# Optimization experiments

Measured on AMD Instinct MI355X. Metric: run time of the kernel, lower is better.

## Reference

```python
import jax, jax.numpy as jnp
import numpy as np

B, F, V, D, K = 16384, 39, 30000, 16, 20
EPS = 1e-5


def bn_eval(x, g, b):
    # inference-mode BatchNorm1d with running_mean=0, running_var=1
    return g * x / jnp.sqrt(1.0 + EPS) + b


def setup_inputs() -> dict:
    key = jax.random.key(0)
    ks = jax.random.split(key, 12)
    x = jax.random.randint(ks[0], (B, F), 0, V)
    emb_table = jax.random.normal(ks[1], (F * V, D), dtype=jnp.float32) * 0.05
    w_c = jax.random.normal(ks[2], (F, F * D), dtype=jnp.float32) * 0.05
    w0 = jax.random.normal(ks[3], (1024, F * D), dtype=jnp.float32) * 0.04
    w1 = jax.random.normal(ks[4], (512, 1024), dtype=jnp.float32) * 0.03
    w_out = jax.random.normal(ks[5], (1, 512), dtype=jnp.float32) * 0.04
    return {
        'x': x, 'emb_table': emb_table,
        'w_c': w_c, 'b_c': jnp.zeros((F,)), 'g_c': jnp.ones((F,)), 'be_c': jnp.zeros((F,)),
        'w0': w0, 'b0': jnp.zeros((1024,)), 'g0': jnp.ones((1024,)), 'be0': jnp.zeros((1024,)),
        'w1': w1, 'b1': jnp.zeros((512,)), 'g1': jnp.ones((512,)), 'be1': jnp.zeros((512,)),
        'w_out': w_out, 'b_out': jnp.zeros((1,)),
    }


def reference(x, emb_table, w_c, b_c, g_c, be_c, w0, b0, g0, be0,
              w1, b1, g1, be1, w_out, b_out):
    offsets = jnp.arange(F, dtype=x.dtype) * V          # per-field offsets
    idx = x + offsets[None, :]                          # [B, F]
    emb = emb_table[idx]                                # [B, F, D] gather

    # controller_mlp: flatten (batch, D, F) layout like torch transpose(1,2)
    flat = jnp.transpose(emb, (0, 2, 1)).reshape(B, F * D)
    h = jax.nn.relu(bn_eval(flat @ w_c.T + b_c, g_c, be_c))
    scores = jax.nn.softmax(h, axis=1)                  # [B, F]

    # kmax_pooling: top-k field indices, sorted ascending, gather weights
    _, kidx = jax.lax.top_k(scores, K)
    kidx = jnp.sort(kidx, axis=1)                       # [B, K]
    w = jnp.take_along_axis(scores, kidx, axis=1)       # [B, K]

    # forward_select: gather selected field embeddings, weight them
    sel = jnp.take_along_axis(emb, kidx[:, :, None], axis=1)  # [B, K, D]
    weighted = sel * w[:, :, None]

    # scatter back into full field slots (unselected fields are zero)
    full = jnp.zeros((B, F, D), weighted.dtype)
    bidx = jnp.arange(B)[:, None]
    full = full.at[bidx, kidx].set(weighted)            # [B, F, D]

    z = jnp.transpose(full, (0, 2, 1)).reshape(B, F * D)
    z = jax.nn.relu(bn_eval(z @ w0.T + b0, g0, be0))
    z = jax.nn.relu(bn_eval(z @ w1.T + b1, g1, be1))
    out = jax.nn.sigmoid(z @ w_out.T + b_out)           # [B, 1]
    return out.squeeze(-1)
```

## Files before the change

kernel.cpp:

```cpp
#include <hip/hip_runtime.h>
#include <math.h>

#define B_SZ 16384
#define F_N 39
#define V_N 30000
#define D_N 16
#define K_SEL 20
#define FD 624
#define KP0 640
#define NCP 64
#define N0 1024
#define N1 512
#define WSL 40

typedef unsigned short u16;
typedef __attribute__((ext_vector_type(8))) short bf16x8;
typedef __attribute__((ext_vector_type(4))) float f32x4;
typedef __attribute__((ext_vector_type(4))) unsigned short u16x4;

__device__ __forceinline__ u16 f2bf(float v) {
    union { float f; unsigned u; } x; x.f = v;
    unsigned r = x.u + 0x7fff + ((x.u >> 16) & 1);
    return (u16)(r >> 16);
}
__device__ __forceinline__ float bf2f(u16 v) {
    union { unsigned u; float f; } x; x.u = ((unsigned)v) << 16;
    return x.f;
}

#define GLD16(gp, lp) __builtin_amdgcn_global_load_lds( \
    (const __attribute__((address_space(1))) unsigned int*)(gp), \
    (__attribute__((address_space(3))) unsigned int*)(lp), 16, 0, 0)

__global__ void convert_kernel(const float* __restrict__ src, u16* __restrict__ dst,
                               int n_el)
{
    int i = blockIdx.x * blockDim.x + threadIdx.x;
    if (i < n_el) dst[i] = f2bf(src[i]);
}

__global__ void prep_w0_kernel(const float* __restrict__ w0, u16* __restrict__ w0p)
{
    int i = blockIdx.x * blockDim.x + threadIdx.x;
    if (i >= N0 * KP0) return;
    int n = i / KP0, kk = i - n * KP0;
    float v = 0.f;
    if (kk < FD) {
        int f = kk >> 4, d = kk & 15;
        v = w0[n * FD + d * F_N + f];
    }
    w0p[i] = f2bf(v);
}

__global__ void prep_wc_kernel(const float* __restrict__ w_c, u16* __restrict__ wcb)
{
    int i = blockIdx.x * blockDim.x + threadIdx.x;
    if (i >= NCP * KP0) return;
    int n = i / KP0, kk = i - n * KP0;
    float v = 0.f;
    if (n < F_N && kk < FD) {
        int f = kk >> 4, d = kk & 15;
        v = w_c[n * FD + d * F_N + f];
    }
    wcb[i] = f2bf(v);
}

__global__ void pad_params_kernel(const float* __restrict__ b_c,
                                  const float* __restrict__ g_c,
                                  const float* __restrict__ be_c,
                                  float* __restrict__ bp, float* __restrict__ gp,
                                  float* __restrict__ bep)
{
    int n = threadIdx.x;
    bp[n]  = (n < F_N) ? b_c[n]  : 0.f;
    gp[n]  = (n < F_N) ? g_c[n]  : 0.f;
    bep[n] = (n < F_N) ? be_c[n] : 0.f;
}

#define GROWS_BLK 64
#define GBLOCKS (B_SZ * F_N / GROWS_BLK)
__global__ __launch_bounds__(256) void gather_kernel(
    const int* __restrict__ x, const float* __restrict__ emb_table,
    u16* __restrict__ flatb)
{
    const int t = threadIdx.x;
    if (blockIdx.x >= GBLOCKS) {
        int b = (blockIdx.x - GBLOCKS) * 256 + t;
        float4 zz = {0.f, 0.f, 0.f, 0.f};
        float4* p = (float4*)(flatb + (size_t)b * KP0 + FD);
        p[0] = zz; p[1] = zz;
        return;
    }
    const int r = blockIdx.x * GROWS_BLK + (t >> 2);
    const int lane4 = t & 3;
    const int b = r / F_N;
    const int f = r - b * F_N;
    const int row = x[r] + f * V_N;
    const float4 v = *(const float4*)(emb_table + (size_t)row * D_N + lane4 * 4);
    u16x4 o = { f2bf(v.x), f2bf(v.y), f2bf(v.z), f2bf(v.w) };
    *(u16x4*)(flatb + (size_t)b * KP0 + f * D_N + lane4 * 4) = o;
}

__global__ __launch_bounds__(256) void controller_gemm_select_kernel(
    const u16* __restrict__ A, const u16* __restrict__ W,
    const float* __restrict__ bias, const float* __restrict__ g,
    const float* __restrict__ be, float* __restrict__ wsel)
{
    __shared__ __align__(16) u16 As[64 * 32];
    __shared__ __align__(16) u16 Bs[64 * 32];
    __shared__ float vv[64][65];

    const int t    = threadIdx.x;
    const int wave = t >> 6;
    const int lane = t & 63;
    const int m0   = blockIdx.x * 64;

    const int lr    = lane >> 2;
    const int swz_u = (lane & 3) ^ ((lane >> 3) & 3);
    const u16* gA = A + (size_t)(m0 + wave * 16 + lr) * KP0 + swz_u * 8;
    const u16* gB = W + (size_t)(wave * 16 + lr) * KP0 + swz_u * 8;
    u16* lA = &As[(wave * 16) * 32];
    u16* lB = &Bs[(wave * 16) * 32];

    const int q    = lane >> 4;
    const int lr16 = lane & 15;

    const int ra = wave * 16 + lr16;
    const int aoff = ra * 32 + ((q ^ ((ra >> 1) & 3)) * 8);
    int boff[4];
    #pragma unroll
    for (int j = 0; j < 4; ++j) {
        int rb = j * 16 + lr16;
        boff[j] = rb * 32 + ((q ^ ((rb >> 1) & 3)) * 8);
    }

    f32x4 acc[4] = {};

    for (int k0 = 0; k0 < KP0; k0 += 32) {
        GLD16(gA, lA); GLD16(gB, lB);
        gA += 32; gB += 32;
        __syncthreads();
        bf16x8 af = *(const bf16x8*)&As[aoff];
        bf16x8 bfr[4];
        #pragma unroll
        for (int j = 0; j < 4; ++j) bfr[j] = *(const bf16x8*)&Bs[boff[j]];
        #pragma unroll
        for (int j = 0; j < 4; ++j)
            acc[j] = __builtin_amdgcn_mfma_f32_16x16x32_bf16(af, bfr[j], acc[j], 0, 0, 0);
        __syncthreads();
    }

    const float rs = rsqrtf(1.0f + 1e-5f);
    #pragma unroll
    for (int j = 0; j < 4; ++j) {
        const int n = j * 16 + lr16;
        const float bn_g = g[n] * rs;
        const float bn_b = be[n];
        const float bi   = bias[n];
        #pragma unroll
        for (int r = 0; r < 4; ++r) {
            float v = acc[j][r] + bi;
            vv[wave * 16 + q * 4 + r][n] = fmaxf(fmaf(bn_g, v, bn_b), 0.f);
        }
    }
    __syncthreads();

    if (t < 64) {
        float rv[F_N];
        #pragma unroll
        for (int f = 0; f < F_N; ++f) rv[f] = vv[t][f];
        float mx = rv[0];
        #pragma unroll
        for (int f = 1; f < F_N; ++f) mx = fmaxf(mx, rv[f]);
        float sum = 0.f;
        #pragma unroll
        for (int f = 0; f < F_N; ++f) { rv[f] = expf(rv[f] - mx); sum += rv[f]; }
        const float inv = 1.f / sum;
        float* wrow = wsel + (size_t)(m0 + t) * WSL;
        #pragma unroll
        for (int f = 0; f < F_N; ++f) {
            int rank = 0;
            #pragma unroll
            for (int gg = 0; gg < F_N; ++gg)
                rank += (rv[gg] > rv[f] || (rv[gg] == rv[f] && gg < f)) ? 1 : 0;
            wrow[f] = (rank < K_SEL) ? rv[f] * inv : 0.f;
        }
    }
}

__global__ __launch_bounds__(256) void select_scale_kernel(
    const u16* __restrict__ flatb, const float* __restrict__ wsel,
    u16* __restrict__ zb)
{
    const int i = blockIdx.x * blockDim.x + threadIdx.x;
    const int b = i / (KP0 / 8);
    const int kk = (i - b * (KP0 / 8)) * 8;
    u16x4 o0 = {0, 0, 0, 0}, o1 = {0, 0, 0, 0};
    if (kk < FD) {
        const float s = wsel[(size_t)b * WSL + (kk >> 4)];
        const u16x4* src = (const u16x4*)(flatb + (size_t)b * KP0 + kk);
        u16x4 a0 = src[0], a1 = src[1];
        o0 = { f2bf(bf2f(a0.x) * s), f2bf(bf2f(a0.y) * s),
               f2bf(bf2f(a0.z) * s), f2bf(bf2f(a0.w) * s) };
        o1 = { f2bf(bf2f(a1.x) * s), f2bf(bf2f(a1.y) * s),
               f2bf(bf2f(a1.z) * s), f2bf(bf2f(a1.w) * s) };
    }
    u16x4* dst = (u16x4*)(zb + (size_t)b * KP0 + kk);
    dst[0] = o0; dst[1] = o1;
}

template<int STORE_BF16>
__global__ __launch_bounds__(256) void gemm_mfma_bn_relu(
    const u16* __restrict__ A, const u16* __restrict__ W,
    const float* __restrict__ bias, const float* __restrict__ g,
    const float* __restrict__ be, void* __restrict__ Cout,
    int M, int N, int Kp)
{
    __shared__ __align__(16) u16 As[128 * 32];
    __shared__ __align__(16) u16 Bs[128 * 32];

    const int t    = threadIdx.x;
    const int wave = t >> 6;
    const int lane = t & 63;
    const int wm   = wave >> 1, wn = wave & 1;
    const int m0   = blockIdx.x * 128;
    const int n0   = blockIdx.y * 128;

    const int lr    = lane >> 2;
    const int swz_u = (lane & 3) ^ ((lane >> 3) & 3);
    const u16* gA0 = A + (size_t)(m0 + wave * 32 + lr) * Kp + swz_u * 8;
    const u16* gA1 = gA0 + 16 * (size_t)Kp;
    const u16* gB0 = W + (size_t)(n0 + wave * 32 + lr) * Kp + swz_u * 8;
    const u16* gB1 = gB0 + 16 * (size_t)Kp;
    u16* lA0 = &As[(wave * 32)      * 32];
    u16* lA1 = &As[(wave * 32 + 16) * 32];
    u16* lB0 = &Bs[(wave * 32)      * 32];
    u16* lB1 = &Bs[(wave * 32 + 16) * 32];

    const int q    = lane >> 4;
    const int lr16 = lane & 15;

    int aoff[4], boff[4];
    #pragma unroll
    for (int i = 0; i < 4; ++i) {
        int ra = wm * 64 + i * 16 + lr16;
        aoff[i] = ra * 32 + ((q ^ ((ra >> 1) & 3)) * 8);
        int rb = wn * 64 + i * 16 + lr16;
        boff[i] = rb * 32 + ((q ^ ((rb >> 1) & 3)) * 8);
    }

    f32x4 acc[4][4] = {};

    for (int k0 = 0; k0 < Kp; k0 += 32) {
        GLD16(gA0, lA0); GLD16(gA1, lA1);
        GLD16(gB0, lB0); GLD16(gB1, lB1);
        gA0 += 32; gA1 += 32; gB0 += 32; gB1 += 32;
        __syncthreads();

        bf16x8 af[4], bfr[4];
        #pragma unroll
        for (int i = 0; i < 4; ++i) af[i]  = *(const bf16x8*)&As[aoff[i]];
        #pragma unroll
        for (int j = 0; j < 4; ++j) bfr[j] = *(const bf16x8*)&Bs[boff[j]];

        #pragma unroll
        for (int i = 0; i < 4; ++i)
            #pragma unroll
            for (int j = 0; j < 4; ++j)
                acc[i][j] = __builtin_amdgcn_mfma_f32_16x16x32_bf16(
                    af[i], bfr[j], acc[i][j], 0, 0, 0);
        __syncthreads();
    }

    const float rs = rsqrtf(1.0f + 1e-5f);
    #pragma unroll
    for (int j = 0; j < 4; ++j) {
        const int n = n0 + wn * 64 + j * 16 + lr16;
        const float bn_g = g[n] * rs;
        const float bn_b = be[n];
        const float bi   = bias[n];
        #pragma unroll
        for (int i = 0; i < 4; ++i) {
            const int mbase = m0 + wm * 64 + i * 16 + q * 4;
            #pragma unroll
            for (int r = 0; r < 4; ++r) {
                float v = acc[i][j][r] + bi;
                v = fmaxf(fmaf(bn_g, v, bn_b), 0.f);
                const size_t off = (size_t)(mbase + r) * N + n;
                if (STORE_BF16) ((u16*)Cout)[off] = f2bf(v);
                else            ((float*)Cout)[off] = v;
            }
        }
    }
}

__global__ __launch_bounds__(256) void out_kernel(
    const u16* __restrict__ h1b, const float* __restrict__ w_out,
    const float* __restrict__ b_out, float* __restrict__ out)
{
    const int wave = threadIdx.x >> 6;
    const int lane = threadIdx.x & 63;
    const int b = blockIdx.x * 4 + wave;
    const u16* row = h1b + (size_t)b * N1;
    float s = 0.f;
    #pragma unroll
    for (int i = 0; i < 8; ++i) {
        int k = lane + i * 64;
        s = fmaf(bf2f(row[k]), w_out[k], s);
    }
    #pragma unroll
    for (int off = 32; off; off >>= 1) s += __shfl_down(s, off, 64);
    if (lane == 0) out[b] = 1.f / (1.f + expf(-(s + b_out[0])));
}

extern "C" void kernel_launch(void* const* d_in, const int* in_sizes, int n_in,
                              void* d_out, int out_size, void* d_ws, size_t ws_size,
                              hipStream_t stream)
{
    const int*   x     = (const int*)  d_in[0];
    const float* emb   = (const float*)d_in[1];
    const float* w_c   = (const float*)d_in[2];
    const float* b_c   = (const float*)d_in[3];
    const float* g_c   = (const float*)d_in[4];
    const float* be_c  = (const float*)d_in[5];
    const float* w0    = (const float*)d_in[6];
    const float* b0    = (const float*)d_in[7];
    const float* g0    = (const float*)d_in[8];
    const float* be0   = (const float*)d_in[9];
    const float* w1    = (const float*)d_in[10];
    const float* b1    = (const float*)d_in[11];
    const float* g1    = (const float*)d_in[12];
    const float* be1   = (const float*)d_in[13];
    const float* w_out = (const float*)d_in[14];
    const float* b_out = (const float*)d_in[15];
    float* out = (float*)d_out;

    u16*   flatb = (u16*)d_ws;
    u16*   zb    = flatb + (size_t)B_SZ * KP0;
    u16*   w0b   = zb    + (size_t)B_SZ * KP0;
    u16*   h0b   = w0b   + (size_t)N0 * KP0;
    u16*   w1b   = h0b   + (size_t)B_SZ * N0;
    u16*   h1b   = w1b   + (size_t)N1 * N0;
    u16*   wcb   = h1b   + (size_t)B_SZ * N1;
    float* wsel  = (float*)(wcb + (size_t)NCP * KP0);
    float* bcp   = wsel + (size_t)B_SZ * WSL;
    float* gcp   = bcp + NCP;
    float* becp  = gcp + NCP;

    pad_params_kernel<<<1, NCP, 0, stream>>>(b_c, g_c, be_c, bcp, gcp, becp);
    prep_wc_kernel<<<(NCP * KP0 + 255) / 256, 256, 0, stream>>>(w_c, wcb);
    prep_w0_kernel<<<(N0 * KP0 + 255) / 256, 256, 0, stream>>>(w0, w0b);
    convert_kernel<<<(N1 * N0 + 255) / 256, 256, 0, stream>>>(w1, w1b, N1 * N0);

    gather_kernel<<<GBLOCKS + B_SZ / 256, 256, 0, stream>>>(x, emb, flatb);

    controller_gemm_select_kernel<<<B_SZ / 64, 256, 0, stream>>>(
        flatb, wcb, bcp, gcp, becp, wsel);

    select_scale_kernel<<<(B_SZ * (KP0 / 8)) / 256, 256, 0, stream>>>(flatb, wsel, zb);

    gemm_mfma_bn_relu<1><<<dim3(B_SZ / 128, N0 / 128), 256, 0, stream>>>(
        zb, w0b, b0, g0, be0, h0b, B_SZ, N0, KP0);
    gemm_mfma_bn_relu<1><<<dim3(B_SZ / 128, N1 / 128), 256, 0, stream>>>(
        h0b, w1b, b1, g1, be1, h1b, B_SZ, N1, N0);

    out_kernel<<<B_SZ / 4, 256, 0, stream>>>(h1b, w_out, b_out, out);
}
```

Before: 255.5 us.

## Fuse embedding gather, controller GEMM, softmax/top-k and scaling into one kernel

Replaces three kernels (gather into flatb, controller GEMM with select, select/scale) with one kernel per 16 batch rows. The kernel gathers embeddings into LDS as bf16, runs the controller MFMA with weights read straight from global memory, then does softmax and rank-based top-k spread across 4 lanes per row and writes the scaled zb. This removes the flatb and wsel round trips and two launches. It also trims the controller N padding from 64 to 48. In exchange, blocks are small single-wave blocks, and each block rereads the wc weights from global/L2 without an LDS tile.

```diff
diff --git a/kernel.cpp b/kernel.cpp
--- a/kernel.cpp
+++ b/kernel.cpp
@@ -8,13 +8,15 @@
 #define K_SEL 20
 #define FD 624
 #define KP0 640
-#define NCP 64
+#define NCP 48
 #define N0 1024
 #define N1 512
-#define WSL 40
+#define CBR 16
+#define ALD 648
 
 typedef unsigned short u16;
 typedef __attribute__((ext_vector_type(8))) short bf16x8;
+typedef __attribute__((ext_vector_type(8))) unsigned short u16x8;
 typedef __attribute__((ext_vector_type(4))) float f32x4;
 typedef __attribute__((ext_vector_type(4))) unsigned short u16x4;
 
@@ -77,136 +79,129 @@
     bep[n] = (n < F_N) ? be_c[n] : 0.f;
 }
 
-#define GROWS_BLK 64
-#define GBLOCKS (B_SZ * F_N / GROWS_BLK)
-__global__ __launch_bounds__(256) void gather_kernel(
+__global__ __launch_bounds__(64) void fused_controller_kernel(
     const int* __restrict__ x, const float* __restrict__ emb_table,
-    u16* __restrict__ flatb)
-{
-    const int t = threadIdx.x;
-    if (blockIdx.x >= GBLOCKS) {
-        int b = (blockIdx.x - GBLOCKS) * 256 + t;
-        float4 zz = {0.f, 0.f, 0.f, 0.f};
-        float4* p = (float4*)(flatb + (size_t)b * KP0 + FD);
-        p[0] = zz; p[1] = zz;
-        return;
-    }
-    const int r = blockIdx.x * GROWS_BLK + (t >> 2);
-    const int lane4 = t & 3;
-    const int b = r / F_N;
-    const int f = r - b * F_N;
-    const int row = x[r] + f * V_N;
-    const float4 v = *(const float4*)(emb_table + (size_t)row * D_N + lane4 * 4);
-    u16x4 o = { f2bf(v.x), f2bf(v.y), f2bf(v.z), f2bf(v.w) };
-    *(u16x4*)(flatb + (size_t)b * KP0 + f * D_N + lane4 * 4) = o;
-}
-
-__global__ __launch_bounds__(256) void controller_gemm_select_kernel(
-    const u16* __restrict__ A, const u16* __restrict__ W,
-    const float* __restrict__ bias, const float* __restrict__ g,
-    const float* __restrict__ be, float* __restrict__ wsel)
-{
-    __shared__ __align__(16) u16 As[64 * 32];
-    __shared__ __align__(16) u16 Bs[64 * 32];
-    __shared__ float vv[64][65];
-
-    const int t    = threadIdx.x;
-    const int wave = t >> 6;
-    const int lane = t & 63;
-    const int m0   = blockIdx.x * 64;
-
-    const int lr    = lane >> 2;
-    const int swz_u = (lane & 3) ^ ((lane >> 3) & 3);
-    const u16* gA = A + (size_t)(m0 + wave * 16 + lr) * KP0 + swz_u * 8;
-    const u16* gB = W + (size_t)(wave * 16 + lr) * KP0 + swz_u * 8;
-    u16* lA = &As[(wave * 16) * 32];
-    u16* lB = &Bs[(wave * 16) * 32];
-
-    const int q    = lane >> 4;
-    const int lr16 = lane & 15;
-
-    const int ra = wave * 16 + lr16;
-    const int aoff = ra * 32 + ((q ^ ((ra >> 1) & 3)) * 8);
-    int boff[4];
-    #pragma unroll
-    for (int j = 0; j < 4; ++j) {
-        int rb = j * 16 + lr16;
-        boff[j] = rb * 32 + ((q ^ ((rb >> 1) & 3)) * 8);
-    }
-
-    f32x4 acc[4] = {};
-
+    const u16* __restrict__ wcb, const float* __restrict__ bcp,
+    const float* __restrict__ gcp, const float* __restrict__ becp,
+    u16* __restrict__ zb)
+{
+    __shared__ __align__(16) u16 Al[CBR * ALD];
+    __shared__ float vv[CBR][49];
+
+    const int lane = threadIdx.x;
+    const int b0   = blockIdx.x * CBR;
+    const int row  = lane >> 2;
+    const int fg   = lane & 3;
+
+    #pragma unroll
+    for (int it = 0; it < 10; ++it) {
+        const int f = fg + 4 * it;
+        if (f < F_N) {
+            const int xi = x[(b0 + row) * F_N + f];
+            const float4* src =
+                (const float4*)(emb_table + (size_t)(xi + f * V_N) * D_N);
+            float4 v0 = src[0], v1 = src[1], v2 = src[2], v3 = src[3];
+            u16x8 o0 = { f2bf(v0.x), f2bf(v0.y), f2bf(v0.z), f2bf(v0.w),
+                         f2bf(v1.x), f2bf(v1.y), f2bf(v1.z), f2bf(v1.w) };
+            u16x8 o1 = { f2bf(v2.x), f2bf(v2.y), f2bf(v2.z), f2bf(v2.w),
+                         f2bf(v3.x), f2bf(v3.y), f2bf(v3.z), f2bf(v3.w) };
+            *(u16x8*)&Al[row * ALD + f * D_N]     = o0;
+            *(u16x8*)&Al[row * ALD + f * D_N + 8] = o1;
+        }
+    }
+    __syncthreads();
+
+    const int m = lane & 15;
+    const int q = lane >> 4;
+    f32x4 acc0 = {}, acc1 = {}, acc2 = {};
+    const u16* ap  = &Al[m * ALD + q * 8];
+    const u16* bp0 = wcb + (size_t)(0  + m) * KP0 + q * 8;
+    const u16* bp1 = wcb + (size_t)(16 + m) * KP0 + q * 8;
+    const u16* bp2 = wcb + (size_t)(32 + m) * KP0 + q * 8;
+    #pragma unroll 4
     for (int k0 = 0; k0 < KP0; k0 += 32) {
-        GLD16(gA, lA); GLD16(gB, lB);
-        gA += 32; gB += 32;
-        __syncthreads();
-        bf16x8 af = *(const bf16x8*)&As[aoff];
-        bf16x8 bfr[4];
-        #pragma unroll
-        for (int j = 0; j < 4; ++j) bfr[j] = *(const bf16x8*)&Bs[boff[j]];
-        #pragma unroll
-        for (int j = 0; j < 4; ++j)
-            acc[j] = __builtin_amdgcn_mfma_f32_16x16x32_bf16(af, bfr[j], acc[j], 0, 0, 0);
-        __syncthreads();
+        bf16x8 af = *(const bf16x8*)ap;
+        bf16x8 b0 = *(const bf16x8*)bp0;
+        bf16x8 b1 = *(const bf16x8*)bp1;
+        bf16x8 b2 = *(const bf16x8*)bp2;
+        acc0 = __builtin_amdgcn_mfma_f32_16x16x32_bf16(af, b0, acc0, 0, 0, 0);
+        acc1 = __builtin_amdgcn_mfma_f32_16x16x32_bf16(af, b1, acc1, 0, 0, 0);
+        acc2 = __builtin_amdgcn_mfma_f32_16x16x32_bf16(af, b2, acc2, 0, 0, 0);
+        ap += 32; bp0 += 32; bp1 += 32; bp2 += 32;
     }
 
     const float rs = rsqrtf(1.0f + 1e-5f);
     #pragma unroll
-    for (int j = 0; j < 4; ++j) {
-        const int n = j * 16 + lr16;
-        const float bn_g = g[n] * rs;
-        const float bn_b = be[n];
-        const float bi   = bias[n];
-        #pragma unroll
-        for (int r = 0; r < 4; ++r) {
-            float v = acc[j][r] + bi;
-            vv[wave * 16 + q * 4 + r][n] = fmaxf(fmaf(bn_g, v, bn_b), 0.f);
+    for (int j = 0; j < 3; ++j) {
+        const f32x4 a = (j == 0) ? acc0 : (j == 1) ? acc1 : acc2;
+        const int n = j * 16 + m;
+        const float gn = gcp[n] * rs;
+        const float bn = becp[n];
+        const float bi = bcp[n];
+        #pragma unroll
+        for (int r = 0; r < 4; ++r)
+            vv[q * 4 + r][n] = fmaxf(fmaf(gn, a[r] + bi, bn), 0.f);
+    }
+    __syncthreads();
+
+    float e[10];
+    float mloc = -1e30f;
+    #pragma unroll
+    for (int it = 0; it < 10; ++it) {
+        const int f = fg + 4 * it;
+        if (f < F_N) { e[it] = vv[row][f]; mloc = fmaxf(mloc, e[it]); }
+    }
+    mloc = fmaxf(mloc, __shfl_xor(mloc, 1, 64));
+    mloc = fmaxf(mloc, __shfl_xor(mloc, 2, 64));
+    float sloc = 0.f;
+    #pragma unroll
+    for (int it = 0; it < 10; ++it) {
+        const int f = fg + 4 * it;
+        if (f < F_N) { e[it] = expf(e[it] - mloc); sloc += e[it]; }
+    }
+    sloc += __shfl_xor(sloc, 1, 64);
+    sloc += __shfl_xor(sloc, 2, 64);
+    const float inv = 1.f / sloc;
+    #pragma unroll
+    for (int it = 0; it < 10; ++it) {
+        const int f = fg + 4 * it;
+        if (f < F_N) vv[row][f] = e[it];
+    }
+    __syncthreads();
+
+    int rank[10] = {};
+    for (int gg = 0; gg < F_N; ++gg) {
+        const float o = vv[row][gg];
+        #pragma unroll
+        for (int it = 0; it < 10; ++it) {
+            const int f = fg + 4 * it;
+            if (f < F_N)
+                rank[it] += (o > e[it] || (o == e[it] && gg < f)) ? 1 : 0;
         }
     }
-    __syncthreads();
-
-    if (t < 64) {
-        float rv[F_N];
-        #pragma unroll
-        for (int f = 0; f < F_N; ++f) rv[f] = vv[t][f];
-        float mx = rv[0];
-        #pragma unroll
-        for (int f = 1; f < F_N; ++f) mx = fmaxf(mx, rv[f]);
-        float sum = 0.f;
-        #pragma unroll
-        for (int f = 0; f < F_N; ++f) { rv[f] = expf(rv[f] - mx); sum += rv[f]; }
-        const float inv = 1.f / sum;
-        float* wrow = wsel + (size_t)(m0 + t) * WSL;
-        #pragma unroll
-        for (int f = 0; f < F_N; ++f) {
-            int rank = 0;
+
+    #pragma unroll
+    for (int it = 0; it < 10; ++it) {
+        const int f = fg + 4 * it;
+        u16* dst = zb + (size_t)(b0 + row) * KP0 + f * D_N;
+        if (f < F_N) {
+            const float w = (rank[it] < K_SEL) ? e[it] * inv : 0.f;
+            u16x8 a0 = *(u16x8*)&Al[row * ALD + f * D_N];
+            u16x8 a1 = *(u16x8*)&Al[row * ALD + f * D_N + 8];
+            u16x8 o0, o1;
             #pragma unroll
-            for (int gg = 0; gg < F_N; ++gg)
-                rank += (rv[gg] > rv[f] || (rv[gg] == rv[f] && gg < f)) ? 1 : 0;
-            wrow[f] = (rank < K_SEL) ? rv[f] * inv : 0.f;
+            for (int k = 0; k < 8; ++k) {
+                o0[k] = f2bf(bf2f(a0[k]) * w);
+                o1[k] = f2bf(bf2f(a1[k]) * w);
+            }
+            *(u16x8*)dst = o0;
+            *(u16x8*)(dst + 8) = o1;
+        } else if (f == F_N) {
+            u16x8 zz = {0, 0, 0, 0, 0, 0, 0, 0};
+            *(u16x8*)dst = zz;
+            *(u16x8*)(dst + 8) = zz;
         }
     }
-}
-
-__global__ __launch_bounds__(256) void select_scale_kernel(
-    const u16* __restrict__ flatb, const float* __restrict__ wsel,
-    u16* __restrict__ zb)
-{
-    const int i = blockIdx.x * blockDim.x + threadIdx.x;
-    const int b = i / (KP0 / 8);
-    const int kk = (i - b * (KP0 / 8)) * 8;
-    u16x4 o0 = {0, 0, 0, 0}, o1 = {0, 0, 0, 0};
-    if (kk < FD) {
-        const float s = wsel[(size_t)b * WSL + (kk >> 4)];
-        const u16x4* src = (const u16x4*)(flatb + (size_t)b * KP0 + kk);
-        u16x4 a0 = src[0], a1 = src[1];
-        o0 = { f2bf(bf2f(a0.x) * s), f2bf(bf2f(a0.y) * s),
-               f2bf(bf2f(a0.z) * s), f2bf(bf2f(a0.w) * s) };
-        o1 = { f2bf(bf2f(a1.x) * s), f2bf(bf2f(a1.y) * s),
-               f2bf(bf2f(a1.z) * s), f2bf(bf2f(a1.w) * s) };
-    }
-    u16x4* dst = (u16x4*)(zb + (size_t)b * KP0 + kk);
-    dst[0] = o0; dst[1] = o1;
 }
 
 template<int STORE_BF16>
@@ -335,15 +330,13 @@
     const float* b_out = (const float*)d_in[15];
     float* out = (float*)d_out;
 
-    u16*   flatb = (u16*)d_ws;
-    u16*   zb    = flatb + (size_t)B_SZ * KP0;
+    u16*   zb    = (u16*)d_ws;
     u16*   w0b   = zb    + (size_t)B_SZ * KP0;
     u16*   h0b   = w0b   + (size_t)N0 * KP0;
     u16*   w1b   = h0b   + (size_t)B_SZ * N0;
     u16*   h1b   = w1b   + (size_t)N1 * N0;
     u16*   wcb   = h1b   + (size_t)B_SZ * N1;
-    float* wsel  = (float*)(wcb + (size_t)NCP * KP0);
-    float* bcp   = wsel + (size_t)B_SZ * WSL;
+    float* bcp   = (float*)(wcb + (size_t)NCP * KP0);
     float* gcp   = bcp + NCP;
     float* becp  = gcp + NCP;
 
@@ -352,12 +345,8 @@
     prep_w0_kernel<<<(N0 * KP0 + 255) / 256, 256, 0, stream>>>(w0, w0b);
     convert_kernel<<<(N1 * N0 + 255) / 256, 256, 0, stream>>>(w1, w1b, N1 * N0);
 
-    gather_kernel<<<GBLOCKS + B_SZ / 256, 256, 0, stream>>>(x, emb, flatb);
-
-    controller_gemm_select_kernel<<<B_SZ / 64, 256, 0, stream>>>(
-        flatb, wcb, bcp, gcp, becp, wsel);
-
-    select_scale_kernel<<<(B_SZ * (KP0 / 8)) / 256, 256, 0, stream>>>(flatb, wsel, zb);
+    fused_controller_kernel<<<B_SZ / CBR, 64, 0, stream>>>(
+        x, emb, wcb, bcp, gcp, becp, zb);
 
     gemm_mfma_bn_relu<1><<<dim3(B_SZ / 128, N0 / 128), 256, 0, stream>>>(
         zb, w0b, b0, g0, be0, h0b, B_SZ, N0, KP0);
```

New measurement: 243.9 us. -4.6%, faster.
